# Kernel optimization log

Measured on AMD Instinct MI355X. Metric: run time of the kernel, lower is better.

Reference implementation:

```python
import jax, jax.numpy as jnp
import numpy as np

D, H, N, BS = 3072, 2048, 16, 512
MAX_LATENT_VAR = 0.1


def setup_inputs() -> dict:
    key = jax.random.key(0)
    ks = jax.random.split(key, 12)
    s = 0.02
    return {
        "x": jax.random.normal(ks[0], (BS, D), dtype=jnp.float32),
        "eps": jax.random.normal(ks[1], (1, BS, N), dtype=jnp.float32),
        "enc_W1": jax.random.normal(ks[2], (D, H), dtype=jnp.float32) * s,
        "enc_b1": jnp.zeros((H,), dtype=jnp.float32),
        "enc_Wmu": jax.random.normal(ks[3], (H, N), dtype=jnp.float32) * s,
        "enc_bmu": jnp.zeros((N,), dtype=jnp.float32),
        "enc_Wls": jax.random.normal(ks[4], (H, 1), dtype=jnp.float32) * s,
        "enc_bls": jnp.zeros((1,), dtype=jnp.float32),
        "dec_W1": jax.random.normal(ks[5], (N, H), dtype=jnp.float32) * 0.1,
        "dec_b1": jnp.zeros((H,), dtype=jnp.float32),
        "dec_W2": jax.random.normal(ks[6], (H, D), dtype=jnp.float32) * s,
        "dec_b2": jnp.zeros((D,), dtype=jnp.float32),
    }


def reference(x, eps, enc_W1, enc_b1, enc_Wmu, enc_bmu, enc_Wls, enc_bls,
              dec_W1, dec_b1, dec_W2, dec_b2):
    bs, Dd = x.shape
    n = dec_W1.shape[0]

    def dec(z):  # smooth 2-layer MLP decoder (supports nested autodiff)
        return jnp.tanh(z @ dec_W1 + dec_b1) @ dec_W2 + dec_b2

    # encoder.forward_with_sigma
    h = jnp.tanh(x @ enc_W1 + enc_b1)
    z_star = h @ enc_Wmu + enc_bmu                      # (bs, n)
    sigma = jnp.exp(h @ enc_Wls + enc_bls)[:, 0]        # (bs,)

    # per-sample Jacobian of decoder: (bs, D, n)
    J = jax.vmap(jax.jacfwd(dec))(z_star)

    # per-sample Hessian of f(z) = stop_grad(d) . d,  d = (x - dec(z)) / sigma
    def f_hess(z, xi, sg):
        d = (xi - dec(z)) / sg
        return jnp.dot(jax.lax.stop_gradient(d), d)
    hess = jax.vmap(jax.hessian(f_hess), in_axes=(0, 0, 0))(z_star, x, sigma)  # (bs,n,n)

    eye = jnp.eye(n, dtype=x.dtype)
    Prec = jnp.einsum('bdi,bdj->bij', J, J) / (sigma ** 2)[:, None, None] + eye + hess

    eigvals = jnp.linalg.eigvalsh(Prec)                 # ascending, (bs, n)
    eigmin = eigvals[:, 0]
    delta = 1.0 / MAX_LATENT_VAR - eigmin               # (bs,)
    Prec = Prec + eye * delta[:, None, None]
    eigvals = eigvals + delta[:, None]

    # upper-triangular Cholesky: U^T U = Prec
    U = jnp.swapaxes(jnp.linalg.cholesky(Prec), -1, -2)  # (bs, n, n)

    def solve1(u, e):  # solve U y = e
        return jax.scipy.linalg.solve_triangular(u, e[:, None], lower=False)[:, 0]
    z_off = jax.vmap(jax.vmap(solve1, in_axes=(0, 0)), in_axes=(None, 0))(U, eps)  # (ne,bs,n)
    z_sample = z_star[None] + z_off

    n_eval = eps.shape[0]
    recon = dec(z_sample.reshape(-1, n)).reshape(n_eval, bs, Dd)
    recon_loss = ((recon - x[None]) ** 2).sum(axis=2).mean(axis=0) / (2.0 * sigma ** 2)
    latent_energy = (z_star ** 2).sum(axis=1) / 2.0 + (1.0 / eigvals).sum(axis=1) / 2.0
    logdet_loss = jnp.log(eigvals).sum(axis=1) / 2.0
    sigma_loss = Dd * jnp.log(sigma)
    neg_log_prob = (recon_loss + latent_energy + logdet_loss + sigma_loss) / Dd
    return (neg_log_prob, recon_loss, latent_energy, logdet_loss, sigma)
```

## Files before the change

### kernel.cpp

```cpp
#include <hip/hip_runtime.h>
#include <hip/hip_bf16.h>
#include <math.h>

#define D_ 3072
#define H_ 2048
#define N_ 16
#define BS_ 512

typedef short s16x8 __attribute__((ext_vector_type(8)));
typedef float f32x4v __attribute__((ext_vector_type(4)));
typedef __hip_bfloat16 bf16;

__device__ __forceinline__ void gload_lds16(const void* g, void* l) {
    __builtin_amdgcn_global_load_lds((const __attribute__((address_space(1))) void*)g,
                                     (__attribute__((address_space(3))) void*)l, 16, 0, 0);
}

__device__ __forceinline__ float bf2f(unsigned short u) {
    unsigned v = (unsigned)u << 16; float f; __builtin_memcpy(&f, &v, 4); return f;
}

__global__ __launch_bounds__(256) void mfma_nt_sk(
    const bf16* __restrict__ A, const bf16* __restrict__ Bt,
    float* __restrict__ C, int M, int N, int K, int KC)
{
    __shared__ __align__(16) bf16 As[128 * 32];
    __shared__ __align__(16) bf16 Bs[128 * 32];
    const int tid = threadIdx.x;
    const int w = tid >> 6, l = tid & 63;
    const int wr = w >> 1, wc = w & 1;
    const int m0 = blockIdx.y * 128, n0 = blockIdx.x * 128;
    const int kbeg = blockIdx.z * KC;

    f32x4v acc[4][4];
    #pragma unroll
    for (int a = 0; a < 4; ++a)
        #pragma unroll
        for (int b = 0; b < 4; ++b) acc[a][b] = (f32x4v){0.f, 0.f, 0.f, 0.f};

    const int srow = l >> 2;
    const int scol = (l & 3) * 8;

    for (int k0 = kbeg; k0 < kbeg + KC; k0 += 32) {
        #pragma unroll
        for (int q = 0; q < 2; ++q) {
            int r0 = w * 32 + q * 16;
            gload_lds16(&A[(size_t)(m0 + r0 + srow) * K + k0 + scol], &As[r0 * 32]);
            gload_lds16(&Bt[(size_t)(n0 + r0 + srow) * K + k0 + scol], &Bs[r0 * 32]);
        }
        __syncthreads();
        s16x8 af[4], bfr[4];
        #pragma unroll
        for (int mf = 0; mf < 4; ++mf)
            af[mf] = *(const s16x8*)&As[(wr * 64 + mf * 16 + (l & 15)) * 32 + (l >> 4) * 8];
        #pragma unroll
        for (int nf = 0; nf < 4; ++nf)
            bfr[nf] = *(const s16x8*)&Bs[(wc * 64 + nf * 16 + (l & 15)) * 32 + (l >> 4) * 8];
        #pragma unroll
        for (int mf = 0; mf < 4; ++mf)
            #pragma unroll
            for (int nf = 0; nf < 4; ++nf)
                acc[mf][nf] = __builtin_amdgcn_mfma_f32_16x16x32_bf16(af[mf], bfr[nf], acc[mf][nf], 0, 0, 0);
        __syncthreads();
    }

    #pragma unroll
    for (int mf = 0; mf < 4; ++mf)
        #pragma unroll
        for (int nf = 0; nf < 4; ++nf) {
            int n = n0 + wc * 64 + nf * 16 + (l & 15);
            #pragma unroll
            for (int r = 0; r < 4; ++r) {
                int m = m0 + wr * 64 + mf * 16 + (l >> 4) * 4 + r;
                atomicAdd(&C[(size_t)m * N + n], acc[mf][nf][r]);
            }
        }
}

__global__ __launch_bounds__(256) void ep_tanh(const float* __restrict__ C,
    const float* __restrict__ bias, float* __restrict__ Hout, int MN, int N)
{
    int base = (blockIdx.x * 256 + threadIdx.x) * 4;
    if (base < MN) {
        float4 c = *(const float4*)&C[base];
        int n = base % N;
        float4 bb = *(const float4*)&bias[n];
        float4 o;
        o.x = tanhf(c.x + bb.x); o.y = tanhf(c.y + bb.y);
        o.z = tanhf(c.z + bb.z); o.w = tanhf(c.w + bb.w);
        *(float4*)&Hout[base] = o;
    }
}

__global__ __launch_bounds__(256) void ep_ebf(const float* __restrict__ C,
    const float* __restrict__ bias, const float* __restrict__ X,
    bf16* __restrict__ Eout, int MN, int N)
{
    int base = (blockIdx.x * 256 + threadIdx.x) * 8;
    if (base < MN) {
        float4 c0 = *(const float4*)&C[base];
        float4 c1 = *(const float4*)&C[base + 4];
        float4 x0 = *(const float4*)&X[base];
        float4 x1 = *(const float4*)&X[base + 4];
        int n = base % N;
        float4 b0 = *(const float4*)&bias[n];
        float4 b1 = *(const float4*)&bias[n + 4];
        union { s16x8 v; bf16 e[8]; } u;
        u.e[0] = __float2bfloat16(x0.x - (c0.x + b0.x));
        u.e[1] = __float2bfloat16(x0.y - (c0.y + b0.y));
        u.e[2] = __float2bfloat16(x0.z - (c0.z + b0.z));
        u.e[3] = __float2bfloat16(x0.w - (c0.w + b0.w));
        u.e[4] = __float2bfloat16(x1.x - (c1.x + b1.x));
        u.e[5] = __float2bfloat16(x1.y - (c1.y + b1.y));
        u.e[6] = __float2bfloat16(x1.z - (c1.z + b1.z));
        u.e[7] = __float2bfloat16(x1.w - (c1.w + b1.w));
        *(s16x8*)&Eout[base] = u.v;
    }
}

__global__ __launch_bounds__(256) void ep_recon(const float* __restrict__ C,
    const float* __restrict__ bias, const float* __restrict__ X, float* __restrict__ rls)
{
    int m = blockIdx.x;
    float s = 0.f;
    for (int n = threadIdx.x * 4; n < D_; n += 1024) {
        float4 c = *(const float4*)&C[(size_t)m * D_ + n];
        float4 bb = *(const float4*)&bias[n];
        float4 xx = *(const float4*)&X[(size_t)m * D_ + n];
        float v0 = c.x + bb.x - xx.x, v1 = c.y + bb.y - xx.y;
        float v2 = c.z + bb.z - xx.z, v3 = c.w + bb.w - xx.w;
        s += v0 * v0 + v1 * v1 + v2 * v2 + v3 * v3;
    }
    __shared__ float red[4];
    int wid = threadIdx.x >> 6, lane = threadIdx.x & 63;
    #pragma unroll
    for (int off = 32; off; off >>= 1) s += __shfl_xor(s, off);
    if (lane == 0) red[wid] = s;
    __syncthreads();
    if (threadIdx.x == 0) rls[m] = red[0] + red[1] + red[2] + red[3];
}

__global__ __launch_bounds__(256) void jtj_fused(
    const bf16* __restrict__ Vt, const bf16* __restrict__ W2t,
    float* __restrict__ S, int Mb, int b0)
{
    __shared__ union {
        struct { __align__(16) bf16 As[128 * 32]; __align__(16) bf16 Bs[128 * 32]; } s;
        __align__(16) bf16 J[128 * 136];
    } u;
    const int tid = threadIdx.x;
    const int w = tid >> 6, l = tid & 63;
    const int wr = w >> 1, wc = w & 1;

    int mb, nb;
    if ((Mb & 7) == 0) {
        int lin = blockIdx.y * 24 + blockIdx.x;
        int xcd = lin & 7, idx = lin >> 3;
        int mchunk = Mb >> 3;
        mb = xcd * mchunk + idx / 24;
        nb = idx % 24;
    } else { mb = blockIdx.y; nb = blockIdx.x; }
    const int m0 = mb * 128, n0 = nb * 128;

    f32x4v acc[4][4];
    #pragma unroll
    for (int a = 0; a < 4; ++a)
        #pragma unroll
        for (int b = 0; b < 4; ++b) acc[a][b] = (f32x4v){0.f, 0.f, 0.f, 0.f};

    const int srow = l >> 2;
    const int scol = (l & 3) * 8;

    for (int k0 = 0; k0 < H_; k0 += 32) {
        #pragma unroll
        for (int q = 0; q < 2; ++q) {
            int r0 = w * 32 + q * 16;
            gload_lds16(&Vt[(size_t)(m0 + r0 + srow) * H_ + k0 + scol], &u.s.As[r0 * 32]);
            gload_lds16(&W2t[(size_t)(n0 + r0 + srow) * H_ + k0 + scol], &u.s.Bs[r0 * 32]);
        }
        __syncthreads();
        s16x8 af[4], bfr[4];
        #pragma unroll
        for (int mf = 0; mf < 4; ++mf)
            af[mf] = *(const s16x8*)&u.s.As[(wr * 64 + mf * 16 + (l & 15)) * 32 + (l >> 4) * 8];
        #pragma unroll
        for (int nf = 0; nf < 4; ++nf)
            bfr[nf] = *(const s16x8*)&u.s.Bs[(wc * 64 + nf * 16 + (l & 15)) * 32 + (l >> 4) * 8];
        #pragma unroll
        for (int mf = 0; mf < 4; ++mf)
            #pragma unroll
            for (int nf = 0; nf < 4; ++nf)
                acc[mf][nf] = __builtin_amdgcn_mfma_f32_16x16x32_bf16(af[mf], bfr[nf], acc[mf][nf], 0, 0, 0);
        __syncthreads();
    }

    __syncthreads();
    #pragma unroll
    for (int mf = 0; mf < 4; ++mf) {
        int rbase = wr * 64 + mf * 16 + (l >> 4) * 4;
        #pragma unroll
        for (int nf = 0; nf < 4; ++nf) {
            int col = wc * 64 + nf * 16 + (l & 15);
            #pragma unroll
            for (int r = 0; r < 4; ++r)
                u.J[(rbase + r) * 136 + col] = __float2bfloat16(acc[mf][nf][r]);
        }
    }
    __syncthreads();

    #pragma unroll
    for (int t2 = 0; t2 < 2; ++t2) {
        int bl = w * 2 + t2;
        f32x4v sp = (f32x4v){0.f, 0.f, 0.f, 0.f};
        #pragma unroll
        for (int kq = 0; kq < 4; ++kq) {
            s16x8 fr = *(const s16x8*)&u.J[(bl * 16 + (l & 15)) * 136 + kq * 32 + (l >> 4) * 8];
            sp = __builtin_amdgcn_mfma_f32_16x16x32_bf16(fr, fr, sp, 0, 0, 0);
        }
        int bglob = b0 + mb * 8 + bl;
        #pragma unroll
        for (int r = 0; r < 4; ++r)
            atomicAdd(&S[(size_t)bglob * 256 + ((l >> 4) * 4 + r) * 16 + (l & 15)], sp[r]);
    }
}

__global__ __launch_bounds__(256) void hess_mfma(const float* __restrict__ t,
    const float* __restrict__ g, const bf16* __restrict__ W1b, float* __restrict__ S)
{
    const int w = threadIdx.x >> 6, l = threadIdx.x & 63;
    const int b = blockIdx.x * 4 + w;
    const int row = l & 15, kq = (l >> 4) * 8;

    f32x4v sp = (f32x4v){0.f, 0.f, 0.f, 0.f};
    for (int k0 = 0; k0 < H_; k0 += 32) {
        int kk = k0 + kq;
        s16x8 wf = *(const s16x8*)&W1b[(size_t)row * H_ + kk];
        float4 t0 = *(const float4*)&t[(size_t)b * H_ + kk];
        float4 t1 = *(const float4*)&t[(size_t)b * H_ + kk + 4];
        float4 g0 = *(const float4*)&g[(size_t)b * H_ + kk];
        float4 g1 = *(const float4*)&g[(size_t)b * H_ + kk + 4];
        float wv[8];
        wv[0] = 2.f * g0.x * t0.x * (1.f - t0.x * t0.x);
        wv[1] = 2.f * g0.y * t0.y * (1.f - t0.y * t0.y);
        wv[2] = 2.f * g0.z * t0.z * (1.f - t0.z * t0.z);
        wv[3] = 2.f * g0.w * t0.w * (1.f - t0.w * t0.w);
        wv[4] = 2.f * g1.x * t1.x * (1.f - t1.x * t1.x);
        wv[5] = 2.f * g1.y * t1.y * (1.f - t1.y * t1.y);
        wv[6] = 2.f * g1.z * t1.z * (1.f - t1.z * t1.z);
        wv[7] = 2.f * g1.w * t1.w * (1.f - t1.w * t1.w);
        union { s16x8 v; bf16 e[8]; } af;
        #pragma unroll
        for (int e = 0; e < 8; ++e)
            af.e[e] = __float2bfloat16(wv[e] * bf2f((unsigned short)wf[e]));
        sp = __builtin_amdgcn_mfma_f32_16x16x32_bf16(af.v, wf, sp, 0, 0, 0);
    }
    #pragma unroll
    for (int r = 0; r < 4; ++r)
        S[(size_t)b * 256 + ((l >> 4) * 4 + r) * 16 + (l & 15)] += sp[r];
}

__global__ __launch_bounds__(256) void cast_bf(const float* __restrict__ in, bf16* __restrict__ out, int n8)
{
    int i = blockIdx.x * 256 + threadIdx.x;
    if (i < n8) {
        const float4* p = (const float4*)in + (size_t)i * 2;
        float4 a = p[0], b = p[1];
        union { s16x8 v; bf16 e[8]; } u;
        u.e[0] = __float2bfloat16(a.x); u.e[1] = __float2bfloat16(a.y);
        u.e[2] = __float2bfloat16(a.z); u.e[3] = __float2bfloat16(a.w);
        u.e[4] = __float2bfloat16(b.x); u.e[5] = __float2bfloat16(b.y);
        u.e[6] = __float2bfloat16(b.z); u.e[7] = __float2bfloat16(b.w);
        *(s16x8*)&out[(size_t)i * 8] = u.v;
    }
}

__global__ __launch_bounds__(256) void castT(const float* __restrict__ in, bf16* __restrict__ out, int R, int C)
{
    __shared__ float tile[64][65];
    int r0 = blockIdx.x * 64, c0 = blockIdx.y * 64;
    int tx = threadIdx.x & 63, ty = threadIdx.x >> 6;
    #pragma unroll
    for (int k = 0; k < 16; ++k) {
        int rr = ty * 16 + k;
        tile[rr][tx] = in[(size_t)(r0 + rr) * C + c0 + tx];
    }
    __syncthreads();
    #pragma unroll
    for (int k = 0; k < 16; ++k) {
        int cc = ty * 16 + k;
        out[(size_t)(c0 + cc) * R + r0 + tx] = __float2bfloat16(tile[tx][cc]);
    }
}

__global__ __launch_bounds__(256) void zsig_kernel(const float* __restrict__ h,
    const float* __restrict__ Wmu, const float* __restrict__ bmu,
    const float* __restrict__ Wls, const float* __restrict__ bls,
    float* __restrict__ z_star, float* __restrict__ lsig, float* __restrict__ sigma)
{
    const int b = blockIdx.x, tid = threadIdx.x;
    float acc[17];
    #pragma unroll
    for (int i = 0; i < 17; ++i) acc[i] = 0.f;
    for (int hh = tid; hh < H_; hh += 256) {
        float hv = h[(size_t)b * H_ + hh];
        const float* wr = &Wmu[(size_t)hh * 16];
        #pragma unroll
        for (int i = 0; i < 16; ++i) acc[i] += hv * wr[i];
        acc[16] += hv * Wls[hh];
    }
    __shared__ float red[17][4];
    const int wid = tid >> 6, lane = tid & 63;
    #pragma unroll
    for (int i = 0; i < 17; ++i) {
        float v = acc[i];
        #pragma unroll
        for (int off = 32; off; off >>= 1) v += __shfl_xor(v, off);
        if (lane == 0) red[i][wid] = v;
    }
    __syncthreads();
    if (tid < 17) {
        float v = red[tid][0] + red[tid][1] + red[tid][2] + red[tid][3];
        if (tid < 16) z_star[(size_t)b * 16 + tid] = v + bmu[tid];
        else { float ls = v + bls[0]; lsig[b] = ls; sigma[b] = expf(ls); }
    }
}

__global__ __launch_bounds__(256) void build_t(const float* __restrict__ z,
    const float* __restrict__ W1, const float* __restrict__ b1,
    float* __restrict__ tf, bf16* __restrict__ tb)
{
    __shared__ float zs[16];
    int b = blockIdx.x, tid = threadIdx.x;
    if (tid < 16) zs[tid] = z[(size_t)b * 16 + tid];
    __syncthreads();
    for (int hh = tid; hh < H_; hh += 256) {
        float a = b1[hh];
        #pragma unroll
        for (int i = 0; i < 16; ++i) a += zs[i] * W1[(size_t)i * H_ + hh];
        float tv = tanhf(a);
        if (tf) tf[(size_t)b * H_ + hh] = tv;
        tb[(size_t)b * H_ + hh] = __float2bfloat16(tv);
    }
}

__global__ __launch_bounds__(256) void build_vt(const float* __restrict__ t,
    const float* __restrict__ W1, bf16* __restrict__ Vt, int b0)
{
    int bl = blockIdx.x, b = b0 + bl, tid = threadIdx.x;
    __shared__ float u[H_];
    for (int hh = tid; hh < H_; hh += 256) {
        float tv = t[(size_t)b * H_ + hh];
        u[hh] = 1.f - tv * tv;
    }
    __syncthreads();
    size_t base = (size_t)bl * 16 * H_;
    int hh = tid * 8;
    for (int i = 0; i < 16; ++i) {
        union { s16x8 v; bf16 e[8]; } pk;
        #pragma unroll
        for (int k = 0; k < 8; ++k)
            pk.e[k] = __float2bfloat16(u[hh + k] * W1[(size_t)i * H_ + hh + k]);
        *(s16x8*)&Vt[base + (size_t)i * H_ + hh] = pk.v;
    }
}

__global__ __launch_bounds__(64) void solve_kernel(const float* __restrict__ S,
    const float* __restrict__ sigma, const float* __restrict__ z_star,
    const float* __restrict__ eps, float* __restrict__ z_sample, float* __restrict__ d_out)
{
    const int lane = threadIdx.x;
    const int q = lane >> 4;
    const int j = lane & 15;
    const int b = blockIdx.x * 4 + q;

    const float sg = sigma[b];
    const float inv_s2 = 1.0f / (sg * sg);

    float a0[16], a[16];
    #pragma unroll
    for (int r = 0; r < 16; ++r) {
        a0[r] = S[(size_t)b * 256 + r * 16 + j] * inv_s2 + ((r == j) ? 1.0f : 0.0f);
        a[r] = a0[r];
    }

    #pragma unroll
    for (int k = 0; k < 14; ++k) {
        float x[16];
        #pragma unroll
        for (int r = 0; r < 16; ++r) x[r] = __shfl(a[k], r, 16);
        float sig2 = 0.f;
        #pragma unroll
        for (int r = 0; r < 16; ++r) if (r > k + 1) sig2 += x[r] * x[r];
        float x0 = x[k + 1];
        float normx = sqrtf(sig2 + x0 * x0);
        float alpha = (x0 >= 0.f) ? -normx : normx;
        float v[16];
        #pragma unroll
        for (int r = 0; r < 16; ++r)
            v[r] = (r <= k) ? 0.f : ((r == k + 1) ? x0 - alpha : x[r]);
        float vtv = 0.f;
        #pragma unroll
        for (int r = 0; r < 16; ++r) vtv += v[r] * v[r];
        float beta = (vtv > 1e-28f) ? 2.0f / vtv : 0.f;
        float sj = 0.f;
        #pragma unroll
        for (int r = 0; r < 16; ++r) sj += a[r] * v[r];
        float av[16];
        #pragma unroll
        for (int r = 0; r < 16; ++r) av[r] = __shfl(sj, r, 16);
        float vtav = 0.f;
        #pragma unroll
        for (int r = 0; r < 16; ++r) vtav += v[r] * av[r];
        float c = 0.5f * beta * vtav;
        float wv[16];
        #pragma unroll
        for (int r = 0; r < 16; ++r) wv[r] = beta * (av[r] - c * v[r]);
        float vj = (j <= k) ? 0.f : ((j == k + 1) ? a[k] - alpha : a[k]);
        float wj = beta * (sj - c * vj);
        #pragma unroll
        for (int r = 0; r < 16; ++r) a[r] -= v[r] * wj + wv[r] * vj;
    }

    float dg[16], eo[15];
    #pragma unroll
    for (int r = 0; r < 16; ++r) dg[r] = __shfl(a[r], r, 16);
    #pragma unroll
    for (int r = 0; r < 15; ++r) eo[r] = __shfl(a[r + 1], r, 16);

    float lo = 1e30f, hi = 1e30f;
    #pragma unroll
    for (int r = 0; r < 16; ++r) {
        float rad = ((r > 0) ? fabsf(eo[r - 1]) : 0.f) + ((r < 15) ? fabsf(eo[r]) : 0.f);
        lo = fminf(lo, dg[r] - rad);
        hi = fminf(hi, dg[r]);
    }
    lo -= 1e-4f; hi += 1e-4f;

    #pragma unroll
    for (int pass = 0; pass < 5; ++pass) {
        float step = (hi - lo) * (1.0f / 17.0f);
        float s = lo + step * (float)(j + 1);
        float qq = dg[0] - s;
        int cnt = (qq < 0.f) ? 1 : 0;
        #pragma unroll
        for (int i = 1; i < 16; ++i) {
            float denom = (fabsf(qq) < 1e-30f) ? -1e-30f : qq;
            qq = dg[i] - s - eo[i - 1] * eo[i - 1] / denom;
            cnt += (qq < 0.f) ? 1 : 0;
        }
        unsigned long long bal = __ballot(cnt >= 1);
        unsigned grp = (unsigned)((bal >> (q * 16)) & 0xffffull);
        int f = grp ? (__ffs(grp) - 1) : 16;
        float nlo = lo + step * (float)f;
        float nhi = (f < 16) ? (lo + step * (float)(f + 1)) : hi;
        lo = nlo; hi = nhi;
    }
    const float lam_min = 0.5f * (lo + hi);
    const float delta = 10.0f - lam_min;

    float bm[16];
    #pragma unroll
    for (int r = 0; r < 16; ++r) bm[r] = a0[r] + ((r == j) ? delta : 0.f);

    float ldsum = 0.f;
    #pragma unroll
    for (int kk = 0; kk < 16; ++kk) {
        float ck[16];
        #pragma unroll
        for (int r = 0; r < 16; ++r) ck[r] = __shfl(bm[kk], r, 16);
        float dkk = sqrtf(fmaxf(ck[kk], 1e-30f));
        float inv = 1.0f / dkk;
        ldsum += logf(dkk);
        float lfull[16];
        #pragma unroll
        for (int r = 0; r < 16; ++r) lfull[r] = ck[r] * inv;
        float lj = bm[kk] * inv;
        if (j == kk) {
            #pragma unroll
            for (int r = 0; r < 16; ++r) bm[r] = (r >= kk) ? lfull[r] : 0.f;
        } else if (j > kk) {
            #pragma unroll
            for (int r = 0; r < 16; ++r)
                if (r > kk) bm[r] -= lfull[r] * lj;
        }
    }

    float w[16];
    #pragma unroll
    for (int r = 0; r < 16; ++r) w[r] = 0.f;
    #pragma unroll
    for (int i = 0; i < 16; ++i) {
        float row[16];
        #pragma unroll
        for (int kx = 0; kx < 16; ++kx) row[kx] = __shfl(bm[i], kx, 16);
        float sacc = 0.f;
        #pragma unroll
        for (int kx = 0; kx < 16; ++kx) if (kx < i) sacc += row[kx] * w[kx];
        float invd = 1.0f / row[i];
        float val = (i == j) ? invd : (-sacc * invd);
        w[i] = (i >= j) ? val : 0.f;
    }

    float tsum = 0.f;
    #pragma unroll
    for (int r = 0; r < 16; ++r) tsum += w[r] * w[r];
    float zv = z_star[(size_t)b * 16 + j];
    float ep = eps[(size_t)b * 16 + j];
    float epsv[16];
    #pragma unroll
    for (int r = 0; r < 16; ++r) epsv[r] = __shfl(ep, r, 16);
    float zoff = 0.f;
    #pragma unroll
    for (int r = 0; r < 16; ++r) zoff += w[r] * epsv[r];
    z_sample[(size_t)b * 16 + j] = zv + zoff;

    float zsq = zv * zv;
    #pragma unroll
    for (int off = 1; off < 16; off <<= 1) {
        tsum += __shfl_xor(tsum, off);
        zsq  += __shfl_xor(zsq, off);
    }
    if (j == 0) {
        d_out[2 * 512 + b] = 0.5f * zsq + 0.5f * tsum;
        d_out[3 * 512 + b] = ldsum;
        d_out[4 * 512 + b] = sg;
    }
}

__global__ void finalize_kernel(const float* __restrict__ rlsum, const float* __restrict__ sigma,
    const float* __restrict__ lsig, float* __restrict__ d_out)
{
    int b = blockIdx.x * 256 + threadIdx.x;
    if (b < BS_) {
        float sg = sigma[b];
        float rl = rlsum[b] / (2.0f * sg * sg);
        float le = d_out[2 * 512 + b];
        float ld = d_out[3 * 512 + b];
        d_out[b] = (rl + le + ld) / 3072.0f + lsig[b];
        d_out[512 + b] = rl;
    }
}

extern "C" void kernel_launch(void* const* d_in, const int* in_sizes, int n_in,
                              void* d_out, int out_size, void* d_ws, size_t ws_size,
                              hipStream_t stream)
{
    const float* x       = (const float*)d_in[0];
    const float* eps     = (const float*)d_in[1];
    const float* enc_W1  = (const float*)d_in[2];
    const float* enc_b1  = (const float*)d_in[3];
    const float* enc_Wmu = (const float*)d_in[4];
    const float* enc_bmu = (const float*)d_in[5];
    const float* enc_Wls = (const float*)d_in[6];
    const float* enc_bls = (const float*)d_in[7];
    const float* dec_W1  = (const float*)d_in[8];
    const float* dec_b1  = (const float*)d_in[9];
    const float* dec_W2  = (const float*)d_in[10];
    const float* dec_b2  = (const float*)d_in[11];
    float* out = (float*)d_out;

    char* wsb = (char*)d_ws;
    size_t off = 0;
    auto alloc = [&](size_t bytes) -> void* {
        off = (off + 255) & ~(size_t)255;
        void* p = wsb + off;
        off += bytes;
        return p;
    };

    float* h    = (float*)alloc((size_t)BS_ * H_ * 4);
    float* t    = (float*)alloc((size_t)BS_ * H_ * 4);
    float* g    = (float*)alloc((size_t)BS_ * H_ * 4);
    float* z_st = (float*)alloc((size_t)BS_ * 16 * 4);
    float* lsig = (float*)alloc(BS_ * 4);
    float* sigm = (float*)alloc(BS_ * 4);
    float* z_sm = (float*)alloc((size_t)BS_ * 16 * 4);
    float* rls  = (float*)alloc(BS_ * 4);
    float* S    = (float*)alloc((size_t)BS_ * 256 * 4);
    float* Ch   = (float*)alloc((size_t)BS_ * H_ * 4);
    float* Cd   = (float*)alloc((size_t)BS_ * D_ * 4);
    bf16* x_bf  = (bf16*)alloc((size_t)BS_ * D_ * 2);
    bf16* eW1t  = (bf16*)alloc((size_t)H_ * D_ * 2);
    bf16* W2b   = (bf16*)alloc((size_t)H_ * D_ * 2);
    bf16* W2t   = (bf16*)alloc((size_t)D_ * H_ * 2);
    bf16* W1b   = (bf16*)alloc((size_t)N_ * H_ * 2);
    bf16* t_bf  = (bf16*)alloc((size_t)BS_ * H_ * 2);
    bf16* e_bf  = (bf16*)alloc((size_t)BS_ * D_ * 2);
    bf16* t2b   = (bf16*)alloc((size_t)BS_ * H_ * 2);

    int nb = 0;
    size_t base_off = off;
    const int cand[3] = {512, 128, 32};
    bf16* Vt = nullptr;
    for (int ci = 0; ci < 3; ++ci) {
        off = base_off;
        int n = cand[ci];
        bf16* vt = (bf16*)alloc((size_t)n * 16 * H_ * 2);
        if (off <= ws_size) { nb = n; Vt = vt; break; }
    }
    if (nb == 0) return;

    cast_bf<<<dim3((BS_ * D_ / 8 + 255) / 256), 256, 0, stream>>>(x, x_bf, BS_ * D_ / 8);
    castT<<<dim3(D_ / 64, H_ / 64), 256, 0, stream>>>(enc_W1, eW1t, D_, H_);
    cast_bf<<<dim3((H_ * D_ / 8 + 255) / 256), 256, 0, stream>>>(dec_W2, W2b, H_ * D_ / 8);
    castT<<<dim3(H_ / 64, D_ / 64), 256, 0, stream>>>(dec_W2, W2t, H_, D_);
    cast_bf<<<dim3((N_ * H_ / 8 + 255) / 256), 256, 0, stream>>>(dec_W1, W1b, N_ * H_ / 8);

    hipMemsetAsync(Ch, 0, (size_t)BS_ * H_ * 4, stream);
    hipMemsetAsync(Cd, 0, (size_t)BS_ * D_ * 4, stream);
    hipMemsetAsync(g,  0, (size_t)BS_ * H_ * 4, stream);
    hipMemsetAsync(S,  0, (size_t)BS_ * 256 * 4, stream);

    mfma_nt_sk<<<dim3(H_ / 128, BS_ / 128, 4), 256, 0, stream>>>(
        x_bf, eW1t, Ch, BS_, H_, D_, D_ / 4);
    ep_tanh<<<dim3(BS_ * H_ / 4 / 256), 256, 0, stream>>>(Ch, enc_b1, h, BS_ * H_, H_);
    zsig_kernel<<<dim3(BS_), 256, 0, stream>>>(h, enc_Wmu, enc_bmu, enc_Wls, enc_bls, z_st, lsig, sigm);
    build_t<<<dim3(BS_), 256, 0, stream>>>(z_st, dec_W1, dec_b1, t, t_bf);
    mfma_nt_sk<<<dim3(D_ / 128, BS_ / 128, 4), 256, 0, stream>>>(
        t_bf, W2t, Cd, BS_, D_, H_, H_ / 4);
    ep_ebf<<<dim3(BS_ * D_ / 8 / 256), 256, 0, stream>>>(Cd, dec_b2, x, e_bf, BS_ * D_, D_);
    mfma_nt_sk<<<dim3(H_ / 128, BS_ / 128, 4), 256, 0, stream>>>(
        e_bf, W2b, g, BS_, H_, D_, D_ / 4);

    for (int b0 = 0; b0 < BS_; b0 += nb) {
        build_vt<<<dim3(nb), 256, 0, stream>>>(t, dec_W1, Vt, b0);
        jtj_fused<<<dim3(D_ / 128, nb * 16 / 128), 256, 0, stream>>>(
            Vt, W2t, S, nb * 16 / 128, b0);
    }
    hess_mfma<<<dim3(BS_ / 4), 256, 0, stream>>>(t, g, W1b, S);

    solve_kernel<<<dim3(BS_ / 4), 64, 0, stream>>>(S, sigm, z_st, eps, z_sm, out);
    build_t<<<dim3(BS_), 256, 0, stream>>>(z_sm, dec_W1, dec_b1, nullptr, t2b);
    hipMemsetAsync(Cd, 0, (size_t)BS_ * D_ * 4, stream);
    mfma_nt_sk<<<dim3(D_ / 128, BS_ / 128, 4), 256, 0, stream>>>(
        t2b, W2t, Cd, BS_, D_, H_, H_ / 4);
    ep_recon<<<dim3(BS_), 256, 0, stream>>>(Cd, dec_b2, x, rls);
    finalize_kernel<<<dim3(2), 256, 0, stream>>>(rls, sigm, lsig, out);
}
```

Before: 377.8 us.

## Fuse weight-cast prep kernels, encoder epilogue, and z/t build; merge memsets

The five separate bf16 cast/transpose launches become one prep_all kernel that partitions blocks across tasks, and dec_W2 is read once to produce both its plain and transposed bf16 copies. The tanh epilogue is folded into the z/sigma reduction, which then also builds the decoder hidden activations, so three kernels become one and the h buffer is dropped. Buffers are reordered so that four memsets collapse into one contiguous memset. This cuts launch overhead and redundant global traffic, though tanh is now computed inside a per-sample kernel with less parallelism.

Result: faster. 359.3 us (-4.9%).

```diff
diff --git a/kernel.cpp b/kernel.cpp
--- a/kernel.cpp
+++ b/kernel.cpp
@@ -75,21 +75,6 @@
                 atomicAdd(&C[(size_t)m * N + n], acc[mf][nf][r]);
             }
         }
-}
-
-__global__ __launch_bounds__(256) void ep_tanh(const float* __restrict__ C,
-    const float* __restrict__ bias, float* __restrict__ Hout, int MN, int N)
-{
-    int base = (blockIdx.x * 256 + threadIdx.x) * 4;
-    if (base < MN) {
-        float4 c = *(const float4*)&C[base];
-        int n = base % N;
-        float4 bb = *(const float4*)&bias[n];
-        float4 o;
-        o.x = tanhf(c.x + bb.x); o.y = tanhf(c.y + bb.y);
-        o.z = tanhf(c.z + bb.z); o.w = tanhf(c.w + bb.w);
-        *(float4*)&Hout[base] = o;
-    }
 }
 
 __global__ __launch_bounds__(256) void ep_ebf(const float* __restrict__ C,
@@ -259,56 +244,92 @@
         S[(size_t)b * 256 + ((l >> 4) * 4 + r) * 16 + (l & 15)] += sp[r];
 }
 
-__global__ __launch_bounds__(256) void cast_bf(const float* __restrict__ in, bf16* __restrict__ out, int n8)
-{
-    int i = blockIdx.x * 256 + threadIdx.x;
-    if (i < n8) {
-        const float4* p = (const float4*)in + (size_t)i * 2;
+__global__ __launch_bounds__(256) void prep_all(
+    const float* __restrict__ x, const float* __restrict__ enc_W1,
+    const float* __restrict__ dec_W2, const float* __restrict__ dec_W1,
+    bf16* __restrict__ x_bf, bf16* __restrict__ eW1t,
+    bf16* __restrict__ W2t, bf16* __restrict__ W2b, bf16* __restrict__ W1b)
+{
+    __shared__ float tile[64][65];
+    const int blk = blockIdx.x;
+    const int tid = threadIdx.x;
+    if (blk < 768) {
+        int i = blk * 256 + tid;
+        const float4* p = (const float4*)x + (size_t)i * 2;
         float4 a = p[0], b = p[1];
         union { s16x8 v; bf16 e[8]; } u;
         u.e[0] = __float2bfloat16(a.x); u.e[1] = __float2bfloat16(a.y);
         u.e[2] = __float2bfloat16(a.z); u.e[3] = __float2bfloat16(a.w);
         u.e[4] = __float2bfloat16(b.x); u.e[5] = __float2bfloat16(b.y);
         u.e[6] = __float2bfloat16(b.z); u.e[7] = __float2bfloat16(b.w);
-        *(s16x8*)&out[(size_t)i * 8] = u.v;
-    }
-}
-
-__global__ __launch_bounds__(256) void castT(const float* __restrict__ in, bf16* __restrict__ out, int R, int C)
-{
-    __shared__ float tile[64][65];
-    int r0 = blockIdx.x * 64, c0 = blockIdx.y * 64;
-    int tx = threadIdx.x & 63, ty = threadIdx.x >> 6;
-    #pragma unroll
-    for (int k = 0; k < 16; ++k) {
-        int rr = ty * 16 + k;
-        tile[rr][tx] = in[(size_t)(r0 + rr) * C + c0 + tx];
-    }
-    __syncthreads();
-    #pragma unroll
-    for (int k = 0; k < 16; ++k) {
-        int cc = ty * 16 + k;
-        out[(size_t)(c0 + cc) * R + r0 + tx] = __float2bfloat16(tile[tx][cc]);
-    }
-}
-
-__global__ __launch_bounds__(256) void zsig_kernel(const float* __restrict__ h,
-    const float* __restrict__ Wmu, const float* __restrict__ bmu,
+        *(s16x8*)&x_bf[(size_t)i * 8] = u.v;
+    } else if (blk < 768 + 1536) {
+        int bid = blk - 768;
+        int r0 = (bid % 48) * 64, c0 = (bid / 48) * 64;
+        int tx = tid & 63, ty = tid >> 6;
+        #pragma unroll
+        for (int k = 0; k < 16; ++k) {
+            int rr = ty * 16 + k;
+            tile[rr][tx] = enc_W1[(size_t)(r0 + rr) * H_ + c0 + tx];
+        }
+        __syncthreads();
+        #pragma unroll
+        for (int k = 0; k < 16; ++k) {
+            int cc = ty * 16 + k;
+            eW1t[(size_t)(c0 + cc) * D_ + r0 + tx] = __float2bfloat16(tile[tx][cc]);
+        }
+    } else if (blk < 768 + 3072) {
+        int bid = blk - 768 - 1536;
+        int r0 = (bid % 32) * 64, c0 = (bid / 32) * 64;
+        int tx = tid & 63, ty = tid >> 6;
+        #pragma unroll
+        for (int k = 0; k < 16; ++k) {
+            int rr = ty * 16 + k;
+            float v = dec_W2[(size_t)(r0 + rr) * D_ + c0 + tx];
+            tile[rr][tx] = v;
+            W2b[(size_t)(r0 + rr) * D_ + c0 + tx] = __float2bfloat16(v);
+        }
+        __syncthreads();
+        #pragma unroll
+        for (int k = 0; k < 16; ++k) {
+            int cc = ty * 16 + k;
+            W2t[(size_t)(c0 + cc) * H_ + r0 + tx] = __float2bfloat16(tile[tx][cc]);
+        }
+    } else {
+        int i = (blk - 768 - 3072) * 256 + tid;
+        if (i < N_ * H_ / 8) {
+            const float4* p = (const float4*)dec_W1 + (size_t)i * 2;
+            float4 a = p[0], b = p[1];
+            union { s16x8 v; bf16 e[8]; } u;
+            u.e[0] = __float2bfloat16(a.x); u.e[1] = __float2bfloat16(a.y);
+            u.e[2] = __float2bfloat16(a.z); u.e[3] = __float2bfloat16(a.w);
+            u.e[4] = __float2bfloat16(b.x); u.e[5] = __float2bfloat16(b.y);
+            u.e[6] = __float2bfloat16(b.z); u.e[7] = __float2bfloat16(b.w);
+            *(s16x8*)&W1b[(size_t)i * 8] = u.v;
+        }
+    }
+}
+
+__global__ __launch_bounds__(256) void zsig_t_kernel(const float* __restrict__ Ch,
+    const float* __restrict__ enc_b1, const float* __restrict__ Wmu, const float* __restrict__ bmu,
     const float* __restrict__ Wls, const float* __restrict__ bls,
-    float* __restrict__ z_star, float* __restrict__ lsig, float* __restrict__ sigma)
+    const float* __restrict__ dW1, const float* __restrict__ db1,
+    float* __restrict__ z_star, float* __restrict__ lsig, float* __restrict__ sigma,
+    float* __restrict__ t, bf16* __restrict__ tb)
 {
     const int b = blockIdx.x, tid = threadIdx.x;
     float acc[17];
     #pragma unroll
     for (int i = 0; i < 17; ++i) acc[i] = 0.f;
     for (int hh = tid; hh < H_; hh += 256) {
-        float hv = h[(size_t)b * H_ + hh];
+        float hv = tanhf(Ch[(size_t)b * H_ + hh] + enc_b1[hh]);
         const float* wr = &Wmu[(size_t)hh * 16];
         #pragma unroll
         for (int i = 0; i < 16; ++i) acc[i] += hv * wr[i];
         acc[16] += hv * Wls[hh];
     }
     __shared__ float red[17][4];
+    __shared__ float zs[16];
     const int wid = tid >> 6, lane = tid & 63;
     #pragma unroll
     for (int i = 0; i < 17; ++i) {
@@ -320,14 +341,22 @@
     __syncthreads();
     if (tid < 17) {
         float v = red[tid][0] + red[tid][1] + red[tid][2] + red[tid][3];
-        if (tid < 16) z_star[(size_t)b * 16 + tid] = v + bmu[tid];
+        if (tid < 16) { float z = v + bmu[tid]; zs[tid] = z; z_star[(size_t)b * 16 + tid] = z; }
         else { float ls = v + bls[0]; lsig[b] = ls; sigma[b] = expf(ls); }
     }
+    __syncthreads();
+    for (int hh = tid; hh < H_; hh += 256) {
+        float a = db1[hh];
+        #pragma unroll
+        for (int i = 0; i < 16; ++i) a += zs[i] * dW1[(size_t)i * H_ + hh];
+        float tv = tanhf(a);
+        t[(size_t)b * H_ + hh] = tv;
+        tb[(size_t)b * H_ + hh] = __float2bfloat16(tv);
+    }
 }
 
 __global__ __launch_bounds__(256) void build_t(const float* __restrict__ z,
-    const float* __restrict__ W1, const float* __restrict__ b1,
-    float* __restrict__ tf, bf16* __restrict__ tb)
+    const float* __restrict__ W1, const float* __restrict__ b1, bf16* __restrict__ tb)
 {
     __shared__ float zs[16];
     int b = blockIdx.x, tid = threadIdx.x;
@@ -337,9 +366,7 @@
         float a = b1[hh];
         #pragma unroll
         for (int i = 0; i < 16; ++i) a += zs[i] * W1[(size_t)i * H_ + hh];
-        float tv = tanhf(a);
-        if (tf) tf[(size_t)b * H_ + hh] = tv;
-        tb[(size_t)b * H_ + hh] = __float2bfloat16(tv);
+        tb[(size_t)b * H_ + hh] = __float2bfloat16(tanhf(a));
     }
 }
 
@@ -568,17 +595,18 @@
         return p;
     };
 
-    float* h    = (float*)alloc((size_t)BS_ * H_ * 4);
+    float* Ch   = (float*)alloc((size_t)BS_ * H_ * 4);
+    float* Cd   = (float*)alloc((size_t)BS_ * D_ * 4);
+    float* g    = (float*)alloc((size_t)BS_ * H_ * 4);
+    float* S    = (float*)alloc((size_t)BS_ * 256 * 4);
+    size_t zero_span = (size_t)((char*)(S + BS_ * 256) - (char*)Ch);
+
     float* t    = (float*)alloc((size_t)BS_ * H_ * 4);
-    float* g    = (float*)alloc((size_t)BS_ * H_ * 4);
     float* z_st = (float*)alloc((size_t)BS_ * 16 * 4);
     float* lsig = (float*)alloc(BS_ * 4);
     float* sigm = (float*)alloc(BS_ * 4);
     float* z_sm = (float*)alloc((size_t)BS_ * 16 * 4);
     float* rls  = (float*)alloc(BS_ * 4);
-    float* S    = (float*)alloc((size_t)BS_ * 256 * 4);
-    float* Ch   = (float*)alloc((size_t)BS_ * H_ * 4);
-    float* Cd   = (float*)alloc((size_t)BS_ * D_ * 4);
     bf16* x_bf  = (bf16*)alloc((size_t)BS_ * D_ * 2);
     bf16* eW1t  = (bf16*)alloc((size_t)H_ * D_ * 2);
     bf16* W2b   = (bf16*)alloc((size_t)H_ * D_ * 2);
@@ -600,22 +628,14 @@
     }
     if (nb == 0) return;
 
-    cast_bf<<<dim3((BS_ * D_ / 8 + 255) / 256), 256, 0, stream>>>(x, x_bf, BS_ * D_ / 8);
-    castT<<<dim3(D_ / 64, H_ / 64), 256, 0, stream>>>(enc_W1, eW1t, D_, H_);
-    cast_bf<<<dim3((H_ * D_ / 8 + 255) / 256), 256, 0, stream>>>(dec_W2, W2b, H_ * D_ / 8);
-    castT<<<dim3(H_ / 64, D_ / 64), 256, 0, stream>>>(dec_W2, W2t, H_, D_);
-    cast_bf<<<dim3((N_ * H_ / 8 + 255) / 256), 256, 0, stream>>>(dec_W1, W1b, N_ * H_ / 8);
-
-    hipMemsetAsync(Ch, 0, (size_t)BS_ * H_ * 4, stream);
-    hipMemsetAsync(Cd, 0, (size_t)BS_ * D_ * 4, stream);
-    hipMemsetAsync(g,  0, (size_t)BS_ * H_ * 4, stream);
-    hipMemsetAsync(S,  0, (size_t)BS_ * 256 * 4, stream);
+    prep_all<<<dim3(768 + 3072 + 16), 256, 0, stream>>>(
+        x, enc_W1, dec_W2, dec_W1, x_bf, eW1t, W2t, W2b, W1b);
+    hipMemsetAsync(Ch, 0, zero_span, stream);
 
     mfma_nt_sk<<<dim3(H_ / 128, BS_ / 128, 4), 256, 0, stream>>>(
         x_bf, eW1t, Ch, BS_, H_, D_, D_ / 4);
-    ep_tanh<<<dim3(BS_ * H_ / 4 / 256), 256, 0, stream>>>(Ch, enc_b1, h, BS_ * H_, H_);
-    zsig_kernel<<<dim3(BS_), 256, 0, stream>>>(h, enc_Wmu, enc_bmu, enc_Wls, enc_bls, z_st, lsig, sigm);
-    build_t<<<dim3(BS_), 256, 0, stream>>>(z_st, dec_W1, dec_b1, t, t_bf);
+    zsig_t_kernel<<<dim3(BS_), 256, 0, stream>>>(Ch, enc_b1, enc_Wmu, enc_bmu, enc_Wls, enc_bls,
+        dec_W1, dec_b1, z_st, lsig, sigm, t, t_bf);
     mfma_nt_sk<<<dim3(D_ / 128, BS_ / 128, 4), 256, 0, stream>>>(
         t_bf, W2t, Cd, BS_, D_, H_, H_ / 4);
     ep_ebf<<<dim3(BS_ * D_ / 8 / 256), 256, 0, stream>>>(Cd, dec_b2, x, e_bf, BS_ * D_, D_);
@@ -630,7 +650,7 @@
     hess_mfma<<<dim3(BS_ / 4), 256, 0, stream>>>(t, g, W1b, S);
 
     solve_kernel<<<dim3(BS_ / 4), 64, 0, stream>>>(S, sigm, z_st, eps, z_sm, out);
-    build_t<<<dim3(BS_), 256, 0, stream>>>(z_sm, dec_W1, dec_b1, nullptr, t2b);
+    build_t<<<dim3(BS_), 256, 0, stream>>>(z_sm, dec_W1, dec_b1, t2b);
     hipMemsetAsync(Cd, 0, (size_t)BS_ * D_ * 4, stream);
     mfma_nt_sk<<<dim3(D_ / 128, BS_ / 128, 4), 256, 0, stream>>>(
         t2b, W2t, Cd, BS_, D_, H_, H_ / 4);
```
